# Kernel optimization log

Hardware: AMD Instinct MI355X
Metric: run time of the kernel (lower is better)

The kernel has to match this reference:

```python
import jax, jax.numpy as jnp
import numpy as np

N = 100000   # nodes
E = 600000   # edges
G = 64       # graphs in batch
H = 128      # hidden size
F_NODE = 2
F_EDGE = 7
RH = 500     # reghead size
NEG_SLOPE = 0.01
BN_EPS = 1e-5


def leaky(x):
    return jnp.where(x >= 0, x, NEG_SLOPE * x)


def gine_conv(x, src, dst, edge_attr, edge_W, edge_b, W1, b1, gamma, beta, W2, b2):
    # PyG GINEConv: message = ReLU(x_j + Lin(edge_attr)); sum-aggregate at dst;
    # out = nn((1+eps)*x + aggr) with eps=0; nn = Lin -> BN(train) -> LeakyReLU -> Lin -> LeakyReLU
    e = edge_attr @ edge_W.T + edge_b                 # [E, d_in]
    m = jax.nn.relu(x[src] + e)                       # gather + add + relu
    aggr = jax.ops.segment_sum(m, dst, num_segments=N)
    h = x + aggr
    h = h @ W1.T + b1                                 # [N, H]
    mu = jnp.mean(h, axis=0)
    var = jnp.var(h, axis=0)                          # biased, matches BN training
    h = gamma * (h - mu) * jax.lax.rsqrt(var + BN_EPS) + beta
    h = leaky(h)
    h = h @ W2.T + b2
    return leaky(h)


def setup_inputs() -> dict:
    key = jax.random.key(0)
    ks = jax.random.split(key, 24)

    def lin(k, out_d, in_d):
        s = 1.0 / np.sqrt(in_d)
        k1, k2 = jax.random.split(k)
        return (jax.random.uniform(k1, (out_d, in_d), jnp.float32, -s, s),
                jax.random.uniform(k2, (out_d,), jnp.float32, -s, s))

    x = jax.random.normal(ks[0], (N, F_NODE), jnp.float32)
    edge_index = jax.random.randint(ks[1], (2, E), 0, N, jnp.int32)
    batch = jnp.sort(jax.random.randint(ks[2], (N,), 0, G, jnp.int32))
    edge_attr = jax.random.normal(ks[3], (E, F_EDGE), jnp.float32)

    # layer 0 (in_dim = F_NODE)
    ew0, eb0 = lin(ks[4], F_NODE, F_EDGE)
    w10, b10 = lin(ks[5], H, F_NODE)
    g0, be0 = jnp.ones((H,), jnp.float32), jnp.zeros((H,), jnp.float32)
    w20, b20 = lin(ks[6], H, H)

    # 3 hidden layers, stacked (in_dim = H)
    L = 3
    ewS = jnp.stack([lin(ks[7 + i], H, F_EDGE)[0] for i in range(L)])
    ebS = jnp.stack([lin(jax.random.fold_in(ks[7 + i], 1), H, F_EDGE)[1] for i in range(L)])
    w1S = jnp.stack([lin(ks[10 + i], H, H)[0] for i in range(L)])
    b1S = jnp.stack([lin(jax.random.fold_in(ks[10 + i], 1), H, H)[1] for i in range(L)])
    gS = jnp.ones((L, H), jnp.float32)
    beS = jnp.zeros((L, H), jnp.float32)
    w2S = jnp.stack([lin(ks[13 + i], H, H)[0] for i in range(L)])
    b2S = jnp.stack([lin(jax.random.fold_in(ks[13 + i], 1), H, H)[1] for i in range(L)])

    wr, br = lin(ks[16], RH, H)
    we, be_ = lin(ks[17], 1, RH)

    return {"x": x, "edge_index": edge_index, "batch": batch, "edge_attr": edge_attr,
            "ew0": ew0, "eb0": eb0, "w10": w10, "b10": b10, "g0": g0, "be0": be0,
            "w20": w20, "b20": b20,
            "ewS": ewS, "ebS": ebS, "w1S": w1S, "b1S": b1S, "gS": gS, "beS": beS,
            "w2S": w2S, "b2S": b2S, "wr": wr, "br": br, "we": we, "be_": be_}


def reference(x, edge_index, batch, edge_attr,
              ew0, eb0, w10, b10, g0, be0, w20, b20,
              ewS, ebS, w1S, b1S, gS, beS, w2S, b2S,
              wr, br, we, be_):
    src, dst = edge_index[0], edge_index[1]
    h = gine_conv(x, src, dst, edge_attr, ew0, eb0, w10, b10, g0, be0, w20, b20)
    h = leaky(h)  # outer self.relu; dropout p=0 is identity
    for i in range(ewS.shape[0]):
        h = gine_conv(h, src, dst, edge_attr, ewS[i], ebS[i], w1S[i], b1S[i],
                      gS[i], beS[i], w2S[i], b2S[i])
        h = leaky(h)
    # global_mean_pool
    sums = jax.ops.segment_sum(h, batch, num_segments=G)
    cnt = jax.ops.segment_sum(jnp.ones((h.shape[0],), h.dtype), batch, num_segments=G)
    pooled = sums / jnp.maximum(cnt, 1.0)[:, None]
    # reghead_layers == 2
    r = leaky(pooled @ wr.T + br)
    return r @ we.T + be_
```

## Files before the change

### kernel.cpp

```cpp
#include <hip/hip_runtime.h>

#define NNODES 100000
#define NEDGES 600000
#define NGRAPH 64
#define HID 128
#define RHD 500
#define NB ((NNODES + 255) / 256)
#define EB ((NEDGES + 255) / 256)
#define GG ((NNODES + 63) / 64)

typedef __attribute__((ext_vector_type(8))) short short8;
typedef __attribute__((ext_vector_type(4))) float f32x4;

__device__ __forceinline__ float leaky1(float x) { return x >= 0.0f ? x : 0.01f * x; }

__device__ __forceinline__ void splitf(float a, unsigned short& h, unsigned short& l)
{
    unsigned u = __float_as_uint(a);
    unsigned r = (u + 0x7FFFu + ((u >> 16) & 1u)) & 0xFFFF0000u;
    h = (unsigned short)(r >> 16);
    float res = a - __uint_as_float(r);
    unsigned u2 = __float_as_uint(res);
    l = (unsigned short)((u2 + 0x7FFFu + ((u2 >> 16) & 1u)) >> 16);
}

__global__ __launch_bounds__(256) void hist_kernel(
    const int* __restrict__ ei, int* __restrict__ deg)
{
    int e = blockIdx.x * 256 + threadIdx.x;
    if (e < NEDGES) atomicAdd(&deg[ei[NEDGES + e]], 1);
}

__global__ __launch_bounds__(256) void scan_blk(
    const int* __restrict__ deg, int* __restrict__ incl, int* __restrict__ bsum)
{
    __shared__ int s[256];
    int t = threadIdx.x;
    int n = blockIdx.x * 256 + t;
    int v = (n < NNODES) ? deg[n] : 0;
    int x = v;
    s[t] = x;
    __syncthreads();
    for (int off = 1; off < 256; off <<= 1) {
        int y = (t >= off) ? s[t - off] : 0;
        __syncthreads();
        x += y; s[t] = x;
        __syncthreads();
    }
    if (n < NNODES) incl[n] = x;
    if (t == 255) bsum[blockIdx.x] = x;
}

__global__ __launch_bounds__(512) void scan_bsum(int* __restrict__ bsum, int nblk)
{
    __shared__ int s[512];
    int t = threadIdx.x;
    int v = (t < nblk) ? bsum[t] : 0;
    int x = v;
    s[t] = x;
    __syncthreads();
    for (int off = 1; off < 512; off <<= 1) {
        int y = (t >= off) ? s[t - off] : 0;
        __syncthreads();
        x += y; s[t] = x;
        __syncthreads();
    }
    if (t < nblk) bsum[t] = x - v;
}

__global__ __launch_bounds__(256) void finalize_rp(
    const int* __restrict__ deg, const int* __restrict__ bsum,
    int* __restrict__ rp, int* __restrict__ cursor)
{
    int n = blockIdx.x * 256 + threadIdx.x;
    if (n >= NNODES) return;
    int ig = rp[n] + bsum[blockIdx.x];
    int st = ig - deg[n];
    rp[n] = st;
    cursor[n] = st;
    if (n == NNODES - 1) rp[NNODES] = ig;
}

__global__ __launch_bounds__(256) void scatter_kernel(
    const int* __restrict__ ei, int* __restrict__ cursor, int* __restrict__ eid)
{
    int e = blockIdx.x * 256 + threadIdx.x;
    if (e >= NEDGES) return;
    int d = ei[NEDGES + e];
    int pos = atomicAdd(&cursor[d], 1);
    eid[pos] = e;
}

__global__ __launch_bounds__(256) void seg_sort(
    const int* __restrict__ rp, int* __restrict__ eid)
{
    int n = blockIdx.x * 256 + threadIdx.x;
    if (n >= NNODES) return;
    int beg = rp[n], end = rp[n + 1];
    for (int i = beg + 1; i < end; ++i) {
        int key = eid[i];
        int j = i - 1;
        while (j >= beg && eid[j] > key) { eid[j + 1] = eid[j]; --j; }
        eid[j + 1] = key;
    }
}

__global__ __launch_bounds__(256) void permute_kernel(
    const int* __restrict__ eid, const int* __restrict__ ei,
    const float* __restrict__ ea, int* __restrict__ srcp, float* __restrict__ eap)
{
    int p = blockIdx.x * 256 + threadIdx.x;
    if (p >= NEDGES) return;
    int id = eid[p];
    srcp[p] = ei[id];
    const float* s = ea + (size_t)id * 7;
    float* d = eap + (size_t)p * 7;
#pragma unroll
    for (int k = 0; k < 7; ++k) d[k] = s[k];
}

__global__ __launch_bounds__(256) void wsplit_kernel(
    const float* __restrict__ w, unsigned short* __restrict__ wh,
    unsigned short* __restrict__ wl)
{
    int i = blockIdx.x * 256 + threadIdx.x;
    unsigned short h, l;
    splitf(w[i], h, l);
    wh[i] = h;
    wl[i] = l;
}

__global__ __launch_bounds__(256) void aggregate0_kernel(
    const float* __restrict__ x, const int* __restrict__ rp,
    const int* __restrict__ srcp, const float* __restrict__ eap,
    const float* __restrict__ ew, const float* __restrict__ eb,
    float* __restrict__ aggr2)
{
    int n = blockIdx.x * 256 + threadIdx.x;
    if (n >= NNODES) return;
    float w0[7], w1[7];
#pragma unroll
    for (int k = 0; k < 7; ++k) { w0[k] = ew[k]; w1[k] = ew[7 + k]; }
    float e0b = eb[0], e1b = eb[1];
    float a0 = x[n * 2 + 0], a1 = x[n * 2 + 1];
    int beg = rp[n], end = rp[n + 1];
    for (int e = beg; e < end; ++e) {
        int s = srcp[e];
        const float* ap = eap + (size_t)e * 7;
        float t0 = e0b, t1 = e1b;
#pragma unroll
        for (int k = 0; k < 7; ++k) {
            float av = ap[k];
            t0 = fmaf(av, w0[k], t0);
            t1 = fmaf(av, w1[k], t1);
        }
        a0 += fmaxf(x[s * 2 + 0] + t0, 0.0f);
        a1 += fmaxf(x[s * 2 + 1] + t1, 0.0f);
    }
    aggr2[n * 2 + 0] = a0;
    aggr2[n * 2 + 1] = a1;
}

__global__ __launch_bounds__(256) void aggregate_kernel(
    const float* __restrict__ hin, const int* __restrict__ rp,
    const int* __restrict__ srcp, const float* __restrict__ eap,
    const float* __restrict__ ew, const float* __restrict__ eb,
    float* __restrict__ A)
{
    int lane = threadIdx.x & 63;
    int w = threadIdx.x >> 6;
    int nbase = blockIdx.x * 32 + w * 8;
    float ew0[7], ew1[7];
#pragma unroll
    for (int k = 0; k < 7; ++k) {
        ew0[k] = ew[lane * 7 + k];
        ew1[k] = ew[(lane + 64) * 7 + k];
    }
    float eb0v = eb[lane], eb1v = eb[lane + 64];
    for (int n = nbase; n < nbase + 8; ++n) {
        float a0 = hin[(size_t)n * HID + lane];
        float a1 = hin[(size_t)n * HID + 64 + lane];
        int beg = rp[n], end = rp[n + 1];
        for (int e = beg; e < end; ++e) {
            int s = srcp[e];
            const float* ap = eap + (size_t)e * 7;
            float t0 = eb0v, t1 = eb1v;
#pragma unroll
            for (int k = 0; k < 7; ++k) {
                float av = ap[k];
                t0 = fmaf(av, ew0[k], t0);
                t1 = fmaf(av, ew1[k], t1);
            }
            float x0 = hin[(size_t)s * HID + lane];
            float x1 = hin[(size_t)s * HID + 64 + lane];
            a0 += fmaxf(x0 + t0, 0.0f);
            a1 += fmaxf(x1 + t1, 0.0f);
        }
        float* Ap = A + (size_t)n * HID;
        Ap[lane] = a0;
        Ap[64 + lane] = a1;
    }
}

__global__ __launch_bounds__(256) void gemm1_l0_kernel(
    const float* __restrict__ aggr2,
    const float* __restrict__ w1, const float* __restrict__ b1,
    float* __restrict__ h1)
{
    int n = blockIdx.x * 256 + threadIdx.x;
    if (n >= NNODES) return;
    float x0 = aggr2[n * 2 + 0];
    float x1 = aggr2[n * 2 + 1];
    float4* out4 = (float4*)(h1 + (size_t)n * HID);
    for (int j = 0; j < HID; j += 4) {
        float4 o;
        o.x = fmaf(x1, w1[(j + 0) * 2 + 1], fmaf(x0, w1[(j + 0) * 2 + 0], b1[j + 0]));
        o.y = fmaf(x1, w1[(j + 1) * 2 + 1], fmaf(x0, w1[(j + 1) * 2 + 0], b1[j + 1]));
        o.z = fmaf(x1, w1[(j + 2) * 2 + 1], fmaf(x0, w1[(j + 2) * 2 + 0], b1[j + 2]));
        o.w = fmaf(x1, w1[(j + 3) * 2 + 1], fmaf(x0, w1[(j + 3) * 2 + 0], b1[j + 3]));
        out4[j >> 2] = o;
    }
}

__global__ __launch_bounds__(256) void bn_stats_part(
    const float* __restrict__ h1, float* __restrict__ part)
{
    __shared__ float ls[HID], lq[HID];
    int c = threadIdx.x & 127;
    int half = threadIdx.x >> 7;
    int base = blockIdx.x * 256;
    int end = base + 256; if (end > NNODES) end = NNODES;
    float s = 0.0f, q = 0.0f;
    for (int r = base + half; r < end; r += 2) {
        float v = h1[(size_t)r * HID + c];
        s += v;
        q = fmaf(v, v, q);
    }
    if (half) { ls[c] = s; lq[c] = q; }
    __syncthreads();
    if (!half) {
        s += ls[c]; q += lq[c];
        part[(size_t)blockIdx.x * 256 + c] = s;
        part[(size_t)blockIdx.x * 256 + 128 + c] = q;
    }
}

__global__ __launch_bounds__(64) void bn_finalize(
    const float* __restrict__ part, int nblk,
    const float* __restrict__ gamma, const float* __restrict__ beta,
    float* __restrict__ scsh)
{
    int c = blockIdx.x;
    int lane = threadIdx.x;
    float s = 0.0f, q = 0.0f;
    for (int i = lane; i < nblk; i += 64) {
        s += part[(size_t)i * 256 + c];
        q += part[(size_t)i * 256 + 128 + c];
    }
#pragma unroll
    for (int off = 32; off >= 1; off >>= 1) {
        s += __shfl_down(s, off);
        q += __shfl_down(q, off);
    }
    if (lane == 0) {
        const float invN = 1.0f / (float)NNODES;
        float mu = s * invN;
        float var = fmaf(-mu, mu, q * invN);
        float iv = rsqrtf(var + 1e-5f);
        float sc = gamma[c] * iv;
        scsh[c] = sc;
        scsh[HID + c] = beta[c] - mu * sc;
    }
}

template<int PRE, int POST>
__global__ __launch_bounds__(256) void gemm_mfma(
    const float* __restrict__ Ain, const float* __restrict__ scsh,
    const unsigned short* __restrict__ wh, const unsigned short* __restrict__ wl,
    const float* __restrict__ bias, float* __restrict__ Hout)
{
    __shared__ __align__(16) short lds[16384];
    const int t = threadIdx.x;
    const int mb = blockIdx.x * 64;

    const float4* sc4 = (const float4*)scsh;
    const float4* sh4 = (const float4*)(scsh + HID);

#pragma unroll
    for (int u = 0; u < 4; ++u) {
        int idx = u * 256 + t;
        int row = idx >> 4, sl = idx & 15;
        float4 v0 = make_float4(0.f, 0.f, 0.f, 0.f);
        float4 v1 = make_float4(0.f, 0.f, 0.f, 0.f);
        int gr = mb + row;
        if (gr < NNODES) {
            const float4* p = (const float4*)(Ain + (size_t)gr * HID + sl * 8);
            v0 = p[0]; v1 = p[1];
            if (PRE) {
                float4 c0 = sc4[sl * 2], c1 = sc4[sl * 2 + 1];
                float4 s0 = sh4[sl * 2], s1 = sh4[sl * 2 + 1];
                v0.x = leaky1(fmaf(v0.x, c0.x, s0.x));
                v0.y = leaky1(fmaf(v0.y, c0.y, s0.y));
                v0.z = leaky1(fmaf(v0.z, c0.z, s0.z));
                v0.w = leaky1(fmaf(v0.w, c0.w, s0.w));
                v1.x = leaky1(fmaf(v1.x, c1.x, s1.x));
                v1.y = leaky1(fmaf(v1.y, c1.y, s1.y));
                v1.z = leaky1(fmaf(v1.z, c1.z, s1.z));
                v1.w = leaky1(fmaf(v1.w, c1.w, s1.w));
            }
        }
        unsigned short h[8], l[8];
        splitf(v0.x, h[0], l[0]); splitf(v0.y, h[1], l[1]);
        splitf(v0.z, h[2], l[2]); splitf(v0.w, h[3], l[3]);
        splitf(v1.x, h[4], l[4]); splitf(v1.y, h[5], l[5]);
        splitf(v1.z, h[6], l[6]); splitf(v1.w, h[7], l[7]);
        short8 hv, lv;
#pragma unroll
        for (int e = 0; e < 8; ++e) { hv[e] = (short)h[e]; lv[e] = (short)l[e]; }
        int byt = row * 256 + ((sl ^ (row & 7)) << 4);
        *(short8*)((char*)lds + byt) = hv;
        *(short8*)((char*)lds + 16384 + byt) = lv;
    }
    __syncthreads();

    const int lane = t & 63;
    const int wv = t >> 6;
    const int cl = lane & 15, g = lane >> 4, x = lane & 7;
    const int colbase = wv * 32;

    int aoff[4];
#pragma unroll
    for (int ks = 0; ks < 4; ++ks)
        aoff[ks] = cl * 256 + (((ks * 4 + g) ^ x) << 4);

    const unsigned short* wb_h0 = wh + (size_t)(colbase + cl) * HID + g * 8;
    const unsigned short* wb_h1 = wb_h0 + 16 * HID;
    const unsigned short* wb_l0 = wl + (size_t)(colbase + cl) * HID + g * 8;
    const unsigned short* wb_l1 = wb_l0 + 16 * HID;

    f32x4 acc[4][2];
#pragma unroll
    for (int rt = 0; rt < 4; ++rt) {
        acc[rt][0] = (f32x4){0.f, 0.f, 0.f, 0.f};
        acc[rt][1] = (f32x4){0.f, 0.f, 0.f, 0.f};
    }

#pragma unroll
    for (int ks = 0; ks < 4; ++ks) {
        short8 bh0 = *(const short8*)(wb_h0 + ks * 32);
        short8 bh1 = *(const short8*)(wb_h1 + ks * 32);
        short8 bl0 = *(const short8*)(wb_l0 + ks * 32);
        short8 bl1 = *(const short8*)(wb_l1 + ks * 32);
#pragma unroll
        for (int rt = 0; rt < 4; ++rt) {
            short8 ah = *(const short8*)((const char*)lds + (rt * 4096) + aoff[ks]);
            short8 al = *(const short8*)((const char*)lds + (16384 + rt * 4096) + aoff[ks]);
            acc[rt][0] = __builtin_amdgcn_mfma_f32_16x16x32_bf16(ah, bh0, acc[rt][0], 0, 0, 0);
            acc[rt][1] = __builtin_amdgcn_mfma_f32_16x16x32_bf16(ah, bh1, acc[rt][1], 0, 0, 0);
            acc[rt][0] = __builtin_amdgcn_mfma_f32_16x16x32_bf16(al, bh0, acc[rt][0], 0, 0, 0);
            acc[rt][1] = __builtin_amdgcn_mfma_f32_16x16x32_bf16(al, bh1, acc[rt][1], 0, 0, 0);
            acc[rt][0] = __builtin_amdgcn_mfma_f32_16x16x32_bf16(ah, bl0, acc[rt][0], 0, 0, 0);
            acc[rt][1] = __builtin_amdgcn_mfma_f32_16x16x32_bf16(ah, bl1, acc[rt][1], 0, 0, 0);
        }
    }

    float bj0 = bias[colbase + cl];
    float bj1 = bias[colbase + 16 + cl];
#pragma unroll
    for (int rt = 0; rt < 4; ++rt) {
        int rbase = mb + rt * 16 + g * 4;
#pragma unroll
        for (int r = 0; r < 4; ++r) {
            int grow = rbase + r;
            if (grow < NNODES) {
                float o0 = acc[rt][0][r] + bj0;
                float o1 = acc[rt][1][r] + bj1;
                if (POST) { o0 = leaky1(leaky1(o0)); o1 = leaky1(leaky1(o1)); }
                Hout[(size_t)grow * HID + colbase + cl] = o0;
                Hout[(size_t)grow * HID + colbase + 16 + cl] = o1;
            }
        }
    }
}

__global__ __launch_bounds__(256) void pool_kernel(
    const float* __restrict__ h, const int* __restrict__ batch,
    float* __restrict__ sums, float* __restrict__ cnt)
{
    int c = threadIdx.x & 127;
    int half = threadIdx.x >> 7;
    int base = blockIdx.x * 128 + half * 64;
    if (base >= NNODES) return;
    int end = base + 64; if (end > NNODES) end = NNODES;
    int g = batch[base];
    float acc = 0.0f, k = 0.0f;
    for (int n = base; n < end; ++n) {
        int gn = batch[n];
        if (gn != g) {
            atomicAdd(&sums[g * HID + c], acc);
            if (c == 0) atomicAdd(&cnt[g], k);
            acc = 0.0f; k = 0.0f; g = gn;
        }
        acc += h[(size_t)n * HID + c];
        k += 1.0f;
    }
    atomicAdd(&sums[g * HID + c], acc);
    if (c == 0) atomicAdd(&cnt[g], k);
}

__global__ __launch_bounds__(512) void reghead_kernel(
    const float* __restrict__ sums, const float* __restrict__ cnt,
    const float* __restrict__ wr, const float* __restrict__ br,
    const float* __restrict__ we, const float* __restrict__ be,
    float* __restrict__ out)
{
    __shared__ float pool[8 * HID];
    __shared__ float red[8][8];
    int g0 = blockIdx.x * 8;
    for (int i = threadIdx.x; i < 8 * HID; i += 512) {
        int g = g0 + (i >> 7);
        float c = cnt[g]; c = fmaxf(c, 1.0f);
        pool[i] = sums[g * HID + (i & 127)] / c;
    }
    __syncthreads();
    int j = threadIdx.x;
    float p[8];
#pragma unroll
    for (int g = 0; g < 8; ++g) p[g] = 0.0f;
    if (j < RHD) {
        float accs[8];
        float bjv = br[j];
#pragma unroll
        for (int g = 0; g < 8; ++g) accs[g] = bjv;
        const float4* wr4 = (const float4*)(wr + (size_t)j * HID);
        const float4* pool4 = (const float4*)pool;
        for (int k = 0; k < 32; ++k) {
            float4 w = wr4[k];
#pragma unroll
            for (int g = 0; g < 8; ++g) {
                float4 pv = pool4[g * 32 + k];
                accs[g] = fmaf(w.x, pv.x, accs[g]);
                accs[g] = fmaf(w.y, pv.y, accs[g]);
                accs[g] = fmaf(w.z, pv.z, accs[g]);
                accs[g] = fmaf(w.w, pv.w, accs[g]);
            }
        }
        float wej = we[j];
#pragma unroll
        for (int g = 0; g < 8; ++g) p[g] = leaky1(accs[g]) * wej;
    }
    int lane = threadIdx.x & 63, wid = threadIdx.x >> 6;
#pragma unroll
    for (int g = 0; g < 8; ++g) {
        float v = p[g];
        v += __shfl_down(v, 32); v += __shfl_down(v, 16); v += __shfl_down(v, 8);
        v += __shfl_down(v, 4);  v += __shfl_down(v, 2);  v += __shfl_down(v, 1);
        if (lane == 0) red[g][wid] = v;
    }
    __syncthreads();
    if (threadIdx.x < 8) {
        float sv = be[0];
#pragma unroll
        for (int w = 0; w < 8; ++w) sv += red[threadIdx.x][w];
        out[g0 + threadIdx.x] = sv;
    }
}

extern "C" void kernel_launch(void* const* d_in, const int* in_sizes, int n_in,
                              void* d_out, int out_size, void* d_ws, size_t ws_size,
                              hipStream_t stream)
{
    const float* x     = (const float*)d_in[0];
    const int*   ei    = (const int*)d_in[1];
    const int*   batch = (const int*)d_in[2];
    const float* ea    = (const float*)d_in[3];
    const float* ew0   = (const float*)d_in[4];
    const float* eb0   = (const float*)d_in[5];
    const float* w10   = (const float*)d_in[6];
    const float* b10   = (const float*)d_in[7];
    const float* g0v   = (const float*)d_in[8];
    const float* be0   = (const float*)d_in[9];
    const float* w20   = (const float*)d_in[10];
    const float* b20   = (const float*)d_in[11];
    const float* ewS   = (const float*)d_in[12];
    const float* ebS   = (const float*)d_in[13];
    const float* w1S   = (const float*)d_in[14];
    const float* b1S   = (const float*)d_in[15];
    const float* gS    = (const float*)d_in[16];
    const float* beS   = (const float*)d_in[17];
    const float* w2S   = (const float*)d_in[18];
    const float* b2S   = (const float*)d_in[19];
    const float* wr    = (const float*)d_in[20];
    const float* br    = (const float*)d_in[21];
    const float* we    = (const float*)d_in[22];
    const float* be_   = (const float*)d_in[23];

    float* ws    = (float*)d_ws;
    float* buf0  = ws;
    float* buf1  = buf0 + (size_t)NNODES * HID;
    float* part  = buf1 + (size_t)NNODES * HID;
    float* scsh  = part + (size_t)NB * 256;
    float* sums  = scsh + 256;
    float* cnt   = sums + NGRAPH * HID;
    float* aggr2 = cnt + NGRAPH;
    float* eap   = aggr2 + (size_t)NNODES * 2;
    int*   deg    = (int*)(eap + (size_t)NEDGES * 7);
    int*   cursor = deg + NNODES;
    int*   bsum   = cursor + NNODES;
    int*   rp     = bsum + 512;
    int*   eid    = rp + NNODES + 1;
    int*   srcp   = eid + NEDGES;
    unsigned short* whA = (unsigned short*)(srcp + NEDGES);
    unsigned short* wlA = whA + 7 * 16384;
    float* out   = (float*)d_out;

    hipMemsetAsync(deg, 0, (size_t)NNODES * sizeof(int), stream);
    hist_kernel<<<EB, 256, 0, stream>>>(ei, deg);
    scan_blk<<<NB, 256, 0, stream>>>(deg, rp, bsum);
    scan_bsum<<<1, 512, 0, stream>>>(bsum, NB);
    finalize_rp<<<NB, 256, 0, stream>>>(deg, bsum, rp, cursor);
    scatter_kernel<<<EB, 256, 0, stream>>>(ei, cursor, eid);
    seg_sort<<<NB, 256, 0, stream>>>(rp, eid);
    permute_kernel<<<EB, 256, 0, stream>>>(eid, ei, ea, srcp, eap);

    wsplit_kernel<<<64, 256, 0, stream>>>(w20, whA, wlA);
    for (int i = 0; i < 3; ++i) {
        wsplit_kernel<<<64, 256, 0, stream>>>(w1S + (size_t)i * HID * HID,
            whA + (size_t)(1 + i) * 16384, wlA + (size_t)(1 + i) * 16384);
        wsplit_kernel<<<64, 256, 0, stream>>>(w2S + (size_t)i * HID * HID,
            whA + (size_t)(4 + i) * 16384, wlA + (size_t)(4 + i) * 16384);
    }

    aggregate0_kernel<<<NB, 256, 0, stream>>>(x, rp, srcp, eap, ew0, eb0, aggr2);
    gemm1_l0_kernel<<<NB, 256, 0, stream>>>(aggr2, w10, b10, buf0);
    bn_stats_part<<<NB, 256, 0, stream>>>(buf0, part);
    bn_finalize<<<HID, 64, 0, stream>>>(part, NB, g0v, be0, scsh);
    gemm_mfma<1, 1><<<GG, 256, 0, stream>>>(buf0, scsh, whA, wlA, b20, buf1);

    int cur = 1;
    float* bufs[2] = { buf0, buf1 };
    for (int i = 0; i < 3; ++i) {
        float* hin  = bufs[cur];
        float* hoth = bufs[cur ^ 1];
        aggregate_kernel<<<NNODES / 32, 256, 0, stream>>>(hin, rp, srcp, eap,
            ewS + (size_t)i * HID * 7, ebS + (size_t)i * HID, hoth);
        gemm_mfma<0, 0><<<GG, 256, 0, stream>>>(hoth, scsh,
            whA + (size_t)(1 + i) * 16384, wlA + (size_t)(1 + i) * 16384,
            b1S + (size_t)i * HID, hin);
        bn_stats_part<<<NB, 256, 0, stream>>>(hin, part);
        bn_finalize<<<HID, 64, 0, stream>>>(part, NB,
            gS + (size_t)i * HID, beS + (size_t)i * HID, scsh);
        gemm_mfma<1, 1><<<GG, 256, 0, stream>>>(hin, scsh,
            whA + (size_t)(4 + i) * 16384, wlA + (size_t)(4 + i) * 16384,
            b2S + (size_t)i * HID, hoth);
        cur ^= 1;
    }

    hipMemsetAsync(sums, 0, (size_t)(NGRAPH * HID + NGRAPH) * sizeof(float), stream);
    pool_kernel<<<(NNODES + 127) / 128, 256, 0, stream>>>(bufs[cur], batch, sums, cnt);
    reghead_kernel<<<NGRAPH / 8, 512, 0, stream>>>(sums, cnt, wr, br, we, be_, out);
}
```

Measured before the change: 827.7 us.

## Fuse BN statistics into GEMM epilogue, batch weight splits, unroll edge loop

The BN sum and sum-of-squares are now computed in the first GEMM's epilogue and reduced per block through LDS, which removes the separate bn_stats_part pass over the 100000x128 activation in each hidden layer. The seven weight-split launches are merged into one kernel. The aggregation edge loop is unrolled by two so that more gathers are in flight at once. A third activation buffer is added so the GEMM output is not overwritten while the stats are read, at the cost of extra workspace and register pressure.

After: 693.6 us. 16.2% less time.

```diff
diff --git a/kernel.cpp b/kernel.cpp
--- a/kernel.cpp
+++ b/kernel.cpp
@@ -119,13 +119,20 @@
     for (int k = 0; k < 7; ++k) d[k] = s[k];
 }
 
-__global__ __launch_bounds__(256) void wsplit_kernel(
-    const float* __restrict__ w, unsigned short* __restrict__ wh,
-    unsigned short* __restrict__ wl)
+__global__ __launch_bounds__(256) void wsplit_all(
+    const float* __restrict__ w20, const float* __restrict__ w1S,
+    const float* __restrict__ w2S,
+    unsigned short* __restrict__ wh, unsigned short* __restrict__ wl)
 {
     int i = blockIdx.x * 256 + threadIdx.x;
+    int m = i >> 14;
+    int off = i & 16383;
+    const float* src;
+    if (m == 0) src = w20;
+    else if (m <= 3) src = w1S + (size_t)(m - 1) * 16384;
+    else src = w2S + (size_t)(m - 4) * 16384;
     unsigned short h, l;
-    splitf(w[i], h, l);
+    splitf(src[off], h, l);
     wh[i] = h;
     wl[i] = l;
 }
@@ -181,7 +188,29 @@
         float a0 = hin[(size_t)n * HID + lane];
         float a1 = hin[(size_t)n * HID + 64 + lane];
         int beg = rp[n], end = rp[n + 1];
-        for (int e = beg; e < end; ++e) {
+        int e = beg;
+        for (; e + 2 <= end; e += 2) {
+            int s0 = srcp[e], s1 = srcp[e + 1];
+            const float* ap0 = eap + (size_t)e * 7;
+            float x00 = hin[(size_t)s0 * HID + lane];
+            float x01 = hin[(size_t)s0 * HID + 64 + lane];
+            float x10 = hin[(size_t)s1 * HID + lane];
+            float x11 = hin[(size_t)s1 * HID + 64 + lane];
+            float t00 = eb0v, t01 = eb1v, t10 = eb0v, t11 = eb1v;
+#pragma unroll
+            for (int k = 0; k < 7; ++k) {
+                float av0 = ap0[k], av1 = ap0[7 + k];
+                t00 = fmaf(av0, ew0[k], t00);
+                t01 = fmaf(av0, ew1[k], t01);
+                t10 = fmaf(av1, ew0[k], t10);
+                t11 = fmaf(av1, ew1[k], t11);
+            }
+            a0 += fmaxf(x00 + t00, 0.0f);
+            a1 += fmaxf(x01 + t01, 0.0f);
+            a0 += fmaxf(x10 + t10, 0.0f);
+            a1 += fmaxf(x11 + t11, 0.0f);
+        }
+        if (e < end) {
             int s = srcp[e];
             const float* ap = eap + (size_t)e * 7;
             float t0 = eb0v, t1 = eb1v;
@@ -273,11 +302,12 @@
     }
 }
 
-template<int PRE, int POST>
+template<int PRE, int POST, int BNSTAT>
 __global__ __launch_bounds__(256) void gemm_mfma(
     const float* __restrict__ Ain, const float* __restrict__ scsh,
     const unsigned short* __restrict__ wh, const unsigned short* __restrict__ wl,
-    const float* __restrict__ bias, float* __restrict__ Hout)
+    const float* __restrict__ bias, float* __restrict__ Hout,
+    float* __restrict__ part)
 {
     __shared__ __align__(16) short lds[16384];
     const int t = threadIdx.x;
@@ -366,6 +396,7 @@
 
     float bj0 = bias[colbase + cl];
     float bj1 = bias[colbase + 16 + cl];
+    float s0 = 0.f, q0 = 0.f, s1 = 0.f, q1 = 0.f;
 #pragma unroll
     for (int rt = 0; rt < 4; ++rt) {
         int rbase = mb + rt * 16 + g * 4;
@@ -378,8 +409,24 @@
                 if (POST) { o0 = leaky1(leaky1(o0)); o1 = leaky1(leaky1(o1)); }
                 Hout[(size_t)grow * HID + colbase + cl] = o0;
                 Hout[(size_t)grow * HID + colbase + 16 + cl] = o1;
+                if (BNSTAT) {
+                    s0 += o0; q0 = fmaf(o0, o0, q0);
+                    s1 += o1; q1 = fmaf(o1, o1, q1);
+                }
             }
         }
+    }
+    if (BNSTAT) {
+        __syncthreads();
+        float* red = (float*)lds;
+        red[(colbase + cl) * 4 + g] = s0;
+        red[(colbase + 16 + cl) * 4 + g] = s1;
+        red[512 + (colbase + cl) * 4 + g] = q0;
+        red[512 + (colbase + 16 + cl) * 4 + g] = q1;
+        __syncthreads();
+        int stat = t >> 7, col = t & 127;
+        const float* bp = red + stat * 512 + col * 4;
+        part[(size_t)blockIdx.x * 256 + stat * 128 + col] = bp[0] + bp[1] + bp[2] + bp[3];
     }
 }
 
@@ -498,8 +545,9 @@
     float* ws    = (float*)d_ws;
     float* buf0  = ws;
     float* buf1  = buf0 + (size_t)NNODES * HID;
-    float* part  = buf1 + (size_t)NNODES * HID;
-    float* scsh  = part + (size_t)NB * 256;
+    float* buf2  = buf1 + (size_t)NNODES * HID;
+    float* part  = buf2 + (size_t)NNODES * HID;
+    float* scsh  = part + (size_t)GG * 256;
     float* sums  = scsh + 256;
     float* cnt   = sums + NGRAPH * HID;
     float* aggr2 = cnt + NGRAPH;
@@ -523,40 +571,28 @@
     seg_sort<<<NB, 256, 0, stream>>>(rp, eid);
     permute_kernel<<<EB, 256, 0, stream>>>(eid, ei, ea, srcp, eap);
 
-    wsplit_kernel<<<64, 256, 0, stream>>>(w20, whA, wlA);
-    for (int i = 0; i < 3; ++i) {
-        wsplit_kernel<<<64, 256, 0, stream>>>(w1S + (size_t)i * HID * HID,
-            whA + (size_t)(1 + i) * 16384, wlA + (size_t)(1 + i) * 16384);
-        wsplit_kernel<<<64, 256, 0, stream>>>(w2S + (size_t)i * HID * HID,
-            whA + (size_t)(4 + i) * 16384, wlA + (size_t)(4 + i) * 16384);
-    }
+    wsplit_all<<<448, 256, 0, stream>>>(w20, w1S, w2S, whA, wlA);
 
     aggregate0_kernel<<<NB, 256, 0, stream>>>(x, rp, srcp, eap, ew0, eb0, aggr2);
     gemm1_l0_kernel<<<NB, 256, 0, stream>>>(aggr2, w10, b10, buf0);
     bn_stats_part<<<NB, 256, 0, stream>>>(buf0, part);
     bn_finalize<<<HID, 64, 0, stream>>>(part, NB, g0v, be0, scsh);
-    gemm_mfma<1, 1><<<GG, 256, 0, stream>>>(buf0, scsh, whA, wlA, b20, buf1);
-
-    int cur = 1;
-    float* bufs[2] = { buf0, buf1 };
+    gemm_mfma<1, 1, 0><<<GG, 256, 0, stream>>>(buf0, scsh, whA, wlA, b20, buf1, part);
+
     for (int i = 0; i < 3; ++i) {
-        float* hin  = bufs[cur];
-        float* hoth = bufs[cur ^ 1];
-        aggregate_kernel<<<NNODES / 32, 256, 0, stream>>>(hin, rp, srcp, eap,
-            ewS + (size_t)i * HID * 7, ebS + (size_t)i * HID, hoth);
-        gemm_mfma<0, 0><<<GG, 256, 0, stream>>>(hoth, scsh,
+        aggregate_kernel<<<NNODES / 32, 256, 0, stream>>>(buf1, rp, srcp, eap,
+            ewS + (size_t)i * HID * 7, ebS + (size_t)i * HID, buf2);
+        gemm_mfma<0, 0, 1><<<GG, 256, 0, stream>>>(buf2, scsh,
             whA + (size_t)(1 + i) * 16384, wlA + (size_t)(1 + i) * 16384,
-            b1S + (size_t)i * HID, hin);
-        bn_stats_part<<<NB, 256, 0, stream>>>(hin, part);
-        bn_finalize<<<HID, 64, 0, stream>>>(part, NB,
+            b1S + (size_t)i * HID, buf0, part);
+        bn_finalize<<<HID, 64, 0, stream>>>(part, GG,
             gS + (size_t)i * HID, beS + (size_t)i * HID, scsh);
-        gemm_mfma<1, 1><<<GG, 256, 0, stream>>>(hin, scsh,
+        gemm_mfma<1, 1, 0><<<GG, 256, 0, stream>>>(buf0, scsh,
             whA + (size_t)(4 + i) * 16384, wlA + (size_t)(4 + i) * 16384,
-            b2S + (size_t)i * HID, hoth);
-        cur ^= 1;
+            b2S + (size_t)i * HID, buf1, part);
     }
 
     hipMemsetAsync(sums, 0, (size_t)(NGRAPH * HID + NGRAPH) * sizeof(float), stream);
-    pool_kernel<<<(NNODES + 127) / 128, 256, 0, stream>>>(bufs[cur], batch, sums, cnt);
+    pool_kernel<<<(NNODES + 127) / 128, 256, 0, stream>>>(buf1, batch, sums, cnt);
     reghead_kernel<<<NGRAPH / 8, 512, 0, stream>>>(sums, cnt, wr, br, we, be_, out);
 }
```
